# Kernel tuning notes

Hardware: AMD Instinct MI355X
Metric: run time of the kernel (lower is better)

## Reference

```python
import jax, jax.numpy as jnp
import numpy as np

T, U, I, B, K = 64, 142, 4500, 16384, 10


def setup_inputs() -> dict:
    key = jax.random.key(0)
    k1, k2, k3, k4, k5, k6 = jax.random.split(key, 6)
    q = jax.random.uniform(k1, (T, U, I), dtype=jnp.float32, minval=0.01, maxval=5.0)
    miss = jax.random.uniform(k2, (T, U, I)) < 0.3
    qos_tensor = jnp.where(miss, 0.0, q)
    # user_avg exactly as in __init__: sum over items / count of rated items (clamped >= 1)
    cnt = jnp.clip((qos_tensor > 0).sum(axis=2).astype(jnp.float32), 1.0, None)
    user_avg = qos_tensor.sum(axis=2) / cnt  # [T, U]
    # time-aggregated similarity: random symmetric matrix in [-1, 1]
    s = jax.random.uniform(k3, (U, U), dtype=jnp.float32, minval=-1.0, maxval=1.0)
    user_sim_agg = 0.5 * (s + s.T)
    user_id = jax.random.randint(k4, (B,), 0, U)
    item_id = jax.random.randint(k5, (B,), 0, I)
    time_id = jax.random.randint(k6, (B,), 0, T)
    return {
        "qos_tensor": qos_tensor,
        "user_avg": user_avg,
        "user_sim_agg": user_sim_agg,
        "user_id": user_id,
        "item_id": item_id,
        "time_id": time_id,
        "top_k": K,
    }


def reference(qos_tensor, user_avg, user_sim_agg, user_id, item_id, time_id, top_k):
    num_users = qos_tensor.shape[1]
    avg_u = user_avg[time_id, user_id]                      # [B]
    sim_u = user_sim_agg[user_id]                           # [B, U]
    # ratings of every user for (time_id, item_id): column gather, [B, U]
    u_idx = jnp.arange(num_users)[None, :]
    item_col = qos_tensor[time_id[:, None], u_idx, item_id[:, None]]
    item_rated = item_col > 0                               # [B, U]
    sim_m = jnp.where(item_rated, sim_u, 0.0)
    top_sim, top_user = jax.lax.top_k(sim_m, top_k)         # [B, K]
    top_sim = top_sim / (top_sim.sum(axis=1, keepdims=True) + 1e-8)
    top_sim = jnp.nan_to_num(top_sim)
    # neighbor ratings and neighbor averages
    r_vs = qos_tensor[time_id[:, None], top_user, item_id[:, None]]  # [B, K]
    avg_v = user_avg[time_id[:, None], top_user]                     # [B, K]
    pred = avg_u + (top_sim * (r_vs - avg_v)).sum(axis=1)            # [B]
    return pred
```

## Files before the change

kernel.cpp:

```cpp
#include <hip/hip_runtime.h>
#include <math.h>

#define T_DIM 64
#define U_DIM 142
#define I_DIM 4500
#define I4_DIM 1125
#define B_DIM 16384
#define K_TOP 10
#define U_PAD 144

__global__ __launch_bounds__(256) void k_clear(int4* __restrict__ slotmap4) {
    const int idx = blockIdx.x * 256 + threadIdx.x;
    if (idx < (T_DIM * I_DIM) / 4)
        slotmap4[idx] = make_int4(-1, -1, -1, -1);
}

__global__ __launch_bounds__(256) void k_assign(const int* __restrict__ iid,
                                                const int* __restrict__ tid,
                                                int* __restrict__ slotmap) {
    const int b  = blockIdx.x * 256 + threadIdx.x;
    const int ti = tid[b] * I_DIM + iid[b];
    atomicCAS(&slotmap[ti], -1, b);
}

__global__ __launch_bounds__(256) void k_extract(const float* __restrict__ qos,
                                                 const int* __restrict__ slotmap,
                                                 float* __restrict__ compact) {
    const int i4 = blockIdx.x * 256 + threadIdx.x;
    if (i4 >= I4_DIM) return;
    const int t  = blockIdx.z;
    const int u0 = blockIdx.y * 16;
    const int un = (u0 + 16 <= U_DIM) ? 16 : (U_DIM - u0);

    const int4 ov = ((const int4*)(slotmap + (size_t)t * I_DIM))[i4];
    if ((ov.x & ov.y & ov.z & ov.w) < 0) return;

    const float4* qcol4 = (const float4*)qos + ((size_t)t * U_DIM + u0) * I4_DIM + i4;

    float4 q[16];
#pragma unroll
    for (int j = 0; j < 16; ++j)
        if (j < un) q[j] = qcol4[(size_t)j * I4_DIM];

#pragma unroll
    for (int j = 0; j < 16; ++j) {
        if (j < un) {
            const int u = u0 + j;
            if (ov.x >= 0) compact[(size_t)ov.x * U_PAD + u] = q[j].x;
            if (ov.y >= 0) compact[(size_t)ov.y * U_PAD + u] = q[j].y;
            if (ov.z >= 0) compact[(size_t)ov.z * U_PAD + u] = q[j].z;
            if (ov.w >= 0) compact[(size_t)ov.w * U_PAD + u] = q[j].w;
        }
    }
}

__global__ __launch_bounds__(256) void k_final(
    const float* __restrict__ compact,
    const float* __restrict__ user_avg,
    const float* __restrict__ user_sim,
    const int*   __restrict__ uid,
    const int*   __restrict__ iid,
    const int*   __restrict__ tid,
    const int*   __restrict__ slotmap,
    float*       __restrict__ out)
{
    const int lane = threadIdx.x & 63;
    const int wid  = threadIdx.x >> 6;
    const int b    = blockIdx.x * 4 + wid;

    const int u = uid[b];
    const int i = iid[b];
    const int t = tid[b];
    const int o = slotmap[t * I_DIM + i];

    const float* crow = compact + (size_t)o * U_PAD;
    const float* srow = user_sim + (size_t)u * U_DIM;
    const float* arow = user_avg + (size_t)t * U_DIM;

    float val[3], con[3];
#pragma unroll
    for (int j = 0; j < 3; ++j) {
        const int v = lane + j * 64;
        float sv = -INFINITY, cv = 0.0f;
        if (v < U_DIM) {
            const float rv = crow[v];
            const float av = arow[v];
            const float s  = srow[v];
            sv = (rv > 0.0f) ? s : 0.0f;
            cv = sv * (rv - av);
        }
        val[j] = sv; con[j] = cv;
    }

    float ssum = 0.0f, wsum = 0.0f;
#pragma unroll
    for (int k = 0; k < K_TOP; ++k) {
        float mv = val[0]; float mc = con[0]; int mk = lane;
        if (val[1] > mv) { mv = val[1]; mc = con[1]; mk = lane + 64; }
        if (val[2] > mv) { mv = val[2]; mc = con[2]; mk = lane + 128; }
#pragma unroll
        for (int off = 32; off > 0; off >>= 1) {
            const float ov = __shfl_xor(mv, off, 64);
            const float oc = __shfl_xor(mc, off, 64);
            const int   ok = __shfl_xor(mk, off, 64);
            if (ov > mv || (ov == mv && ok < mk)) { mv = ov; mc = oc; mk = ok; }
        }
        ssum += mv; wsum += mc;
        if ((mk & 63) == lane) {
            const int slot = mk >> 6;
            if (slot == 0)      val[0] = -INFINITY;
            else if (slot == 1) val[1] = -INFINITY;
            else                val[2] = -INFINITY;
        }
    }

    if (lane == 0) out[b] = arow[u] + wsum / (ssum + 1e-8f);
}

__global__ __launch_bounds__(256) void ucf_fallback(
    const float* __restrict__ qos, const float* __restrict__ user_avg,
    const float* __restrict__ user_sim, const int* __restrict__ uid,
    const int* __restrict__ iid, const int* __restrict__ tid,
    float* __restrict__ out)
{
    const int lane = threadIdx.x & 63;
    const int wid  = threadIdx.x >> 6;
    const int b    = blockIdx.x * 4 + wid;
    const int u = uid[b], i = iid[b], t = tid[b];
    const float* qcol = qos + ((size_t)t * U_DIM) * (size_t)I_DIM + i;
    const float* srow = user_sim + (size_t)u * U_DIM;
    const float* arow = user_avg + (size_t)t * U_DIM;
    float val[3], con[3];
#pragma unroll
    for (int j = 0; j < 3; ++j) {
        const int v = lane + j * 64;
        float sv = -INFINITY, cv = 0.0f;
        if (v < U_DIM) {
            const float rv = qcol[(size_t)v * I_DIM];
            sv = (rv > 0.0f) ? srow[v] : 0.0f;
            cv = sv * (rv - arow[v]);
        }
        val[j] = sv; con[j] = cv;
    }
    float ssum = 0.0f, wsum = 0.0f;
#pragma unroll
    for (int k = 0; k < K_TOP; ++k) {
        float mv = val[0]; float mc = con[0]; int mk = lane;
        if (val[1] > mv) { mv = val[1]; mc = con[1]; mk = lane + 64; }
        if (val[2] > mv) { mv = val[2]; mc = con[2]; mk = lane + 128; }
#pragma unroll
        for (int off = 32; off > 0; off >>= 1) {
            const float ov = __shfl_xor(mv, off, 64);
            const float oc = __shfl_xor(mc, off, 64);
            const int   ok = __shfl_xor(mk, off, 64);
            if (ov > mv || (ov == mv && ok < mk)) { mv = ov; mc = oc; mk = ok; }
        }
        ssum += mv; wsum += mc;
        if ((mk & 63) == lane) {
            const int slot = mk >> 6;
            if (slot == 0)      val[0] = -INFINITY;
            else if (slot == 1) val[1] = -INFINITY;
            else                val[2] = -INFINITY;
        }
    }
    if (lane == 0) out[b] = arow[u] + wsum / (ssum + 1e-8f);
}

extern "C" void kernel_launch(void* const* d_in, const int* in_sizes, int n_in,
                              void* d_out, int out_size, void* d_ws, size_t ws_size,
                              hipStream_t stream) {
    const float* qos  = (const float*)d_in[0];
    const float* uavg = (const float*)d_in[1];
    const float* usim = (const float*)d_in[2];
    const int*   uid  = (const int*)d_in[3];
    const int*   iid  = (const int*)d_in[4];
    const int*   tid  = (const int*)d_in[5];
    float* out = (float*)d_out;

    const size_t smap_bytes = (size_t)T_DIM * I_DIM * sizeof(int);
    const size_t off_compact = (smap_bytes + 255) & ~(size_t)255;
    const size_t need = off_compact + (size_t)B_DIM * U_PAD * sizeof(float);

    if (ws_size >= need) {
        int*   slotmap = (int*)d_ws;
        float* compact = (float*)((char*)d_ws + off_compact);

        k_clear  <<<(T_DIM * I_DIM / 4 + 255) / 256, 256, 0, stream>>>((int4*)slotmap);
        k_assign <<<B_DIM / 256,                     256, 0, stream>>>(iid, tid, slotmap);
        dim3 eg((I4_DIM + 255) / 256, (U_DIM + 15) / 16, T_DIM);
        k_extract<<<eg,                              256, 0, stream>>>(qos, slotmap, compact);
        k_final  <<<B_DIM / 4,                       256, 0, stream>>>(compact, uavg, usim,
                                                                       uid, iid, tid, slotmap, out);
    } else {
        ucf_fallback<<<B_DIM / 4, 256, 0, stream>>>(qos, uavg, usim, uid, iid, tid, out);
    }
}
```

Baseline: 301.1 us.

## Stage extracted columns in LDS tile and write compact rows coalesced

The extract kernel now handles a chunk of 128 float4 item groups per block for one time step. It compacts the hit item groups into shared memory and assigns each requested slot a column in an LDS tile of up to 72 rows. Gathered QoS values are scattered into that tile and then written to the compact buffer as contiguous float4 rows, replacing the strided 4-byte global scatter. Slots beyond the cap fall back to direct global writes. In exchange, the grid has fewer blocks, each using about 41KB of LDS, which may reduce occupancy and parallelism.

After: 288.2 us. 4.3% less time.

```diff
diff --git a/kernel.cpp b/kernel.cpp
--- a/kernel.cpp
+++ b/kernel.cpp
@@ -8,6 +8,8 @@
 #define B_DIM 16384
 #define K_TOP 10
 #define U_PAD 144
+#define CHUNK_I4 128
+#define CAP 72
 
 __global__ __launch_bounds__(256) void k_clear(int4* __restrict__ slotmap4) {
     const int idx = blockIdx.x * 256 + threadIdx.x;
@@ -26,31 +28,91 @@
 __global__ __launch_bounds__(256) void k_extract(const float* __restrict__ qos,
                                                  const int* __restrict__ slotmap,
                                                  float* __restrict__ compact) {
-    const int i4 = blockIdx.x * 256 + threadIdx.x;
-    if (i4 >= I4_DIM) return;
-    const int t  = blockIdx.z;
-    const int u0 = blockIdx.y * 16;
-    const int un = (u0 + 16 <= U_DIM) ? 16 : (U_DIM - u0);
-
-    const int4 ov = ((const int4*)(slotmap + (size_t)t * I_DIM))[i4];
-    if ((ov.x & ov.y & ov.z & ov.w) < 0) return;
-
-    const float4* qcol4 = (const float4*)qos + ((size_t)t * U_DIM + u0) * I4_DIM + i4;
-
-    float4 q[16];
-#pragma unroll
-    for (int j = 0; j < 16; ++j)
-        if (j < un) q[j] = qcol4[(size_t)j * I4_DIM];
-
-#pragma unroll
-    for (int j = 0; j < 16; ++j) {
-        if (j < un) {
-            const int u = u0 + j;
-            if (ov.x >= 0) compact[(size_t)ov.x * U_PAD + u] = q[j].x;
-            if (ov.y >= 0) compact[(size_t)ov.y * U_PAD + u] = q[j].y;
-            if (ov.z >= 0) compact[(size_t)ov.z * U_PAD + u] = q[j].z;
-            if (ov.w >= 0) compact[(size_t)ov.w * U_PAD + u] = q[j].w;
-        }
+    __shared__ int  s_nhit, s_ncol;
+    __shared__ int  s_hit_i4[CHUNK_I4];
+    __shared__ int4 s_hit_cols[CHUNK_I4];
+    __shared__ int4 s_hit_own[CHUNK_I4];
+    __shared__ int  s_col_b[CAP];
+    __shared__ __align__(16) float s_tile[CAP * U_PAD];
+
+    const int t   = blockIdx.y;
+    const int c0  = blockIdx.x * CHUNK_I4;
+    const int ni4 = (c0 + CHUNK_I4 <= I4_DIM) ? CHUNK_I4 : (I4_DIM - c0);
+    const int tid = threadIdx.x;
+
+    if (tid == 0) { s_nhit = 0; s_ncol = 0; }
+    __syncthreads();
+
+    if (tid < ni4) {
+        const int4 ov = ((const int4*)(slotmap + (size_t)t * I_DIM))[c0 + tid];
+        if ((ov.x & ov.y & ov.z & ov.w) >= 0) {
+            const int h = atomicAdd(&s_nhit, 1);
+            s_hit_i4[h]  = c0 + tid;
+            s_hit_own[h] = ov;
+            int4 cols;
+            cols.x = (ov.x >= 0) ? atomicAdd(&s_ncol, 1) : -1;
+            cols.y = (ov.y >= 0) ? atomicAdd(&s_ncol, 1) : -1;
+            cols.z = (ov.z >= 0) ? atomicAdd(&s_ncol, 1) : -1;
+            cols.w = (ov.w >= 0) ? atomicAdd(&s_ncol, 1) : -1;
+            s_hit_cols[h] = cols;
+            if (cols.x >= 0 && cols.x < CAP) s_col_b[cols.x] = ov.x;
+            if (cols.y >= 0 && cols.y < CAP) s_col_b[cols.y] = ov.y;
+            if (cols.z >= 0 && cols.z < CAP) s_col_b[cols.z] = ov.z;
+            if (cols.w >= 0 && cols.w < CAP) s_col_b[cols.w] = ov.w;
+        }
+    }
+    __syncthreads();
+
+    const int nhit = s_nhit;
+    const int ncol = (s_ncol < CAP) ? s_ncol : CAP;
+
+    const int lane = tid & 63;
+    const int w    = tid >> 6;
+    const int ustart = w * 36;
+    const int uend   = (ustart + 36 < U_DIM) ? (ustart + 36) : U_DIM;
+
+    for (int hb = 0; hb < nhit; hb += 64) {
+        const int  h   = hb + lane;
+        const bool act = (h < nhit);
+        const int  i4g = act ? s_hit_i4[h] : 0;
+        int4 cols = make_int4(-1, -1, -1, -1);
+        int4 own  = make_int4(0, 0, 0, 0);
+        if (act) { cols = s_hit_cols[h]; own = s_hit_own[h]; }
+        const float4* qb = (const float4*)qos + (size_t)t * U_DIM * I4_DIM + i4g;
+
+        for (int u0 = ustart; u0 < uend; u0 += 4) {
+            const int m = (uend - u0 < 4) ? (uend - u0) : 4;
+            float4 q[4];
+#pragma unroll
+            for (int j = 0; j < 4; ++j)
+                if (act && j < m) q[j] = qb[(size_t)(u0 + j) * I4_DIM];
+#pragma unroll
+            for (int j = 0; j < 4; ++j) {
+                if (act && j < m) {
+                    const int u = u0 + j;
+#define SCATTER(QV, CC, OO)                                                   \
+    if ((CC) >= 0) {                                                          \
+        if ((CC) < CAP) s_tile[(CC) * U_PAD + u] = (QV);                      \
+        else compact[(size_t)(OO) * U_PAD + u] = (QV);                        \
+    }
+                    SCATTER(q[j].x, cols.x, own.x)
+                    SCATTER(q[j].y, cols.y, own.y)
+                    SCATTER(q[j].z, cols.z, own.z)
+                    SCATTER(q[j].w, cols.w, own.w)
+#undef SCATTER
+                }
+            }
+        }
+    }
+    __syncthreads();
+
+    float4* cmp4 = (float4*)compact;
+    const float4* tile4 = (const float4*)s_tile;
+    const int nf = ncol * 36;
+    for (int idx = tid; idx < nf; idx += 256) {
+        const int c = idx / 36;
+        const int f = idx - c * 36;
+        cmp4[(size_t)s_col_b[c] * 36 + f] = tile4[c * 36 + f];
     }
 }
 
@@ -187,7 +249,7 @@
 
         k_clear  <<<(T_DIM * I_DIM / 4 + 255) / 256, 256, 0, stream>>>((int4*)slotmap);
         k_assign <<<B_DIM / 256,                     256, 0, stream>>>(iid, tid, slotmap);
-        dim3 eg((I4_DIM + 255) / 256, (U_DIM + 15) / 16, T_DIM);
+        dim3 eg((I4_DIM + CHUNK_I4 - 1) / CHUNK_I4, T_DIM);
         k_extract<<<eg,                              256, 0, stream>>>(qos, slotmap, compact);
         k_final  <<<B_DIM / 4,                       256, 0, stream>>>(compact, uavg, usim,
                                                                        uid, iid, tid, slotmap, out);
```
